# Kernel optimization log

Hardware: AMD Instinct MI355X
Metric: run time of the kernel (lower is better)

The kernel has to match this reference:

```python
import jax, jax.numpy as jnp
import numpy as np

# dims
A, V = 262, 100000          # alphabet, vocab
EC, HC = 64, 128            # char embed / char lstm hidden
EW, HW = 300, 512           # word embed / word lstm hidden
FC, OUT = 512, 20           # fc dim / num classes
S, L = 2048, 16             # words per sentence, chars per word
DW = EW + 2 * HC            # word-lstm input dim = 556


def _lstm_final(x, Wih, Whh, bih, bhh):
    """Run a unidirectional LSTM over x: [T, B, E]; return final hidden [B, H].
    Gate order (torch): i, f, g, o. c' = sig(f)*c + sig(i)*tanh(g); h = sig(o)*tanh(c')."""
    B = x.shape[1]
    H = Whh.shape[1]
    # precompute input projections for all timesteps: [T, B, 4H]
    xz = jnp.einsum('tbe,ge->tbg', x, Wih) + bih

    def step(carry, xz_t):
        h, c = carry
        z = xz_t + h @ Whh.T + bhh
        i, f, g, o = jnp.split(z, 4, axis=-1)
        c = jax.nn.sigmoid(f) * c + jax.nn.sigmoid(i) * jnp.tanh(g)
        h = jax.nn.sigmoid(o) * jnp.tanh(c)
        return (h, c), None

    init = (jnp.zeros((B, H), x.dtype), jnp.zeros((B, H), x.dtype))
    (h, _), _ = jax.lax.scan(step, init, xz)
    return h


def _bilstm_final(x, pf, pb):
    """Bidirectional LSTM final hidden states, concatenated: [B, 2H].
    Matches torch's hidden_state.view(-1, 2H) for num_layers=1."""
    hf = _lstm_final(x, *pf)
    hb = _lstm_final(x[::-1], *pb)
    return jnp.concatenate([hf, hb], axis=-1)


def setup_inputs() -> dict:
    key = jax.random.key(0)
    ks = jax.random.split(key, 24)
    n = lambda k, shp: (jax.random.normal(k, shp, dtype=jnp.float32) * 0.05)
    inp = {
        'sentence_c': jax.random.randint(ks[0], (S, L), 0, A),
        'sentence_w': jax.random.randint(ks[1], (S,), 0, V),
        'char_emb': n(ks[2], (A, EC)),
        'cWih_f': n(ks[3], (4 * HC, EC)), 'cWhh_f': n(ks[4], (4 * HC, HC)),
        'cbih_f': n(ks[5], (4 * HC,)),    'cbhh_f': n(ks[6], (4 * HC,)),
        'cWih_b': n(ks[7], (4 * HC, EC)), 'cWhh_b': n(ks[8], (4 * HC, HC)),
        'cbih_b': n(ks[9], (4 * HC,)),    'cbhh_b': n(ks[10], (4 * HC,)),
        'word_emb': n(ks[11], (V, EW)),
        'wWih_f': n(ks[12], (4 * HW, DW)), 'wWhh_f': n(ks[13], (4 * HW, HW)),
        'wbih_f': n(ks[14], (4 * HW,)),    'wbhh_f': n(ks[15], (4 * HW,)),
        'wWih_b': n(ks[16], (4 * HW, DW)), 'wWhh_b': n(ks[17], (4 * HW, HW)),
        'wbih_b': n(ks[18], (4 * HW,)),    'wbhh_b': n(ks[19], (4 * HW,)),
        'fc1_w': n(ks[20], (FC, 2 * HW)), 'fc1_b': n(ks[21], (FC,)),
        'fc2_w': n(ks[22], (OUT, FC)),    'fc2_b': n(ks[23], (OUT,)),
    }
    return inp


def reference(sentence_c, sentence_w, char_emb,
              cWih_f, cWhh_f, cbih_f, cbhh_f, cWih_b, cWhh_b, cbih_b, cbhh_b,
              word_emb,
              wWih_f, wWhh_f, wbih_f, wbhh_f, wWih_b, wWhh_b, wbih_b, wbhh_b,
              fc1_w, fc1_b, fc2_w, fc2_b):
    # --- per-word char BiLSTM, batched over all S words at once ---
    ce = char_emb[sentence_c]                 # [S, L, EC]
    ce = jnp.transpose(ce, (1, 0, 2))         # [L, S, EC] : time-major, words as batch
    char_enc = _bilstm_final(ce,
                             (cWih_f, cWhh_f, cbih_f, cbhh_f),
                             (cWih_b, cWhh_b, cbih_b, cbhh_b))  # [S, 2*HC]
    # --- word-level BiLSTM over the sentence (batch 1) ---
    we = word_emb[sentence_w]                 # [S, EW]
    wc = jnp.concatenate([we, char_enc], axis=-1)[:, None, :]   # [S, 1, DW]
    h = _bilstm_final(wc,
                      (wWih_f, wWhh_f, wbih_f, wbhh_f),
                      (wWih_b, wWhh_b, wbih_b, wbhh_b))         # [1, 2*HW]
    # --- classifier head ---
    z = jax.nn.relu(h @ fc1_w.T + fc1_b)
    z = z @ fc2_w.T + fc2_b
    return jax.nn.softmax(z, axis=-1)         # [1, OUT]
```

## Files before the change

kernel.cpp:

```cpp
#include <hip/hip_runtime.h>
#include <math.h>

#define SDIM 2048
#define LDIM 16
#define ECD 64
#define HCD 128
#define EWD 300
#define HWD 512
#define DWD 556
#define FCD 512
#define OUTD 20

typedef unsigned int uint32;

static constexpr int OFF_CWIHT = 0;
static constexpr int OFF_CWHHT = 65536;
static constexpr int OFF_CENC  = 196608;
static constexpr int OFF_WC    = 720896;
static constexpr int OFF_H     = 1859584;
static constexpr int OFF_HFIN  = 3957760;

#define SENT 0xFFFFFFFFu
#define HSLOT 1049088

__device__ __forceinline__ float sigmoidf_(float x) {
    return 1.0f / (1.0f + __expf(-x));
}
__device__ __forceinline__ float tanhf_(float x) {
    x = fminf(10.0f, fmaxf(-10.0f, x));
    float e2 = __expf(2.0f * x);
    return (e2 - 1.0f) / (e2 + 1.0f);
}

__global__ void k0_prep(const float* __restrict__ cWih_f, const float* __restrict__ cWhh_f,
                        const float* __restrict__ cWih_b, const float* __restrict__ cWhh_b,
                        float* __restrict__ ws) {
    const int nt = gridDim.x * blockDim.x;
    const int t0 = blockIdx.x * blockDim.x + threadIdx.x;
    float* cWihT = ws + OFF_CWIHT;
    float* cWhhT = ws + OFF_CWHHT;
    uint32* hT = (uint32*)(ws + OFF_H);
    for (int i = t0; i < 2 * 512 * 64; i += nt) {
        int d = i / (512 * 64), rem = i % (512 * 64);
        int r = rem / 64, k = rem % 64;
        const float* src = d ? cWih_b : cWih_f;
        cWihT[(d * 64 + k) * 512 + r] = src[r * 64 + k];
    }
    for (int i = t0; i < 2 * 512 * 128; i += nt) {
        int d = i / (512 * 128), rem = i % (512 * 128);
        int r = rem / 128, k = rem % 128;
        const float* src = d ? cWhh_b : cWhh_f;
        cWhhT[(d * 128 + k) * 512 + r] = src[r * 128 + k];
    }
    for (int i = t0; i < 2 * HSLOT; i += nt) {
        int rel = i % HSLOT;
        hT[i] = (rel < 512) ? 0u : SENT;
    }
}

__global__ __launch_bounds__(256) void k1_charlstm(
        const int* __restrict__ sc, const float* __restrict__ cemb,
        float* __restrict__ ws,
        const float* __restrict__ cbih_f, const float* __restrict__ cbhh_f,
        const float* __restrict__ cbih_b, const float* __restrict__ cbhh_b) {
    const int tid = threadIdx.x;
    const int dir = blockIdx.x >> 8;
    const int w0 = (blockIdx.x & 255) * 8;
    const float* WihT = ws + OFF_CWIHT + dir * 64 * 512;
    const float* WhhT = ws + OFF_CWHHT + dir * 128 * 512;
    float* char_enc = ws + OFF_CENC;
    const float* bih = dir ? cbih_b : cbih_f;
    const float* bhh = dir ? cbhh_b : cbhh_f;

    __shared__ __align__(16) float x_lds[8][64];
    __shared__ __align__(16) float h_lds[8][128];
    __shared__ float fo_lds[2][8][128];

    const int r0 = tid, r1 = tid + 256;
    const float bz0 = bih[r0] + bhh[r0];
    const float bz1 = bih[r1] + bhh[r1];

    for (int i = tid; i < 8 * 128; i += 256) ((float*)h_lds)[i] = 0.0f;
    float c[8];
#pragma unroll
    for (int w = 0; w < 8; w++) c[w] = 0.0f;
    __syncthreads();

    for (int t = 0; t < 16; t++) {
        const int tx = dir ? (15 - t) : t;
        {
            int w = tid >> 6, e = tid & 63;
            int i0 = sc[(w0 + w) * 16 + tx];
            x_lds[w][e] = cemb[i0 * 64 + e];
            int i1 = sc[(w0 + w + 4) * 16 + tx];
            x_lds[w + 4][e] = cemb[i1 * 64 + e];
        }
        __syncthreads();

        float a0[8], a1[8];
#pragma unroll
        for (int w = 0; w < 8; w++) { a0[w] = bz0; a1[w] = bz1; }

        for (int k = 0; k < 64; k += 4) {
            float w00 = WihT[(k + 0) * 512 + r0], w01 = WihT[(k + 1) * 512 + r0];
            float w02 = WihT[(k + 2) * 512 + r0], w03 = WihT[(k + 3) * 512 + r0];
            float w10 = WihT[(k + 0) * 512 + r1], w11 = WihT[(k + 1) * 512 + r1];
            float w12 = WihT[(k + 2) * 512 + r1], w13 = WihT[(k + 3) * 512 + r1];
#pragma unroll
            for (int w = 0; w < 8; w++) {
                float4 xq = *(const float4*)&x_lds[w][k];
                a0[w] += w00 * xq.x + w01 * xq.y + w02 * xq.z + w03 * xq.w;
                a1[w] += w10 * xq.x + w11 * xq.y + w12 * xq.z + w13 * xq.w;
            }
        }
        for (int k = 0; k < 128; k += 4) {
            float w00 = WhhT[(k + 0) * 512 + r0], w01 = WhhT[(k + 1) * 512 + r0];
            float w02 = WhhT[(k + 2) * 512 + r0], w03 = WhhT[(k + 3) * 512 + r0];
            float w10 = WhhT[(k + 0) * 512 + r1], w11 = WhhT[(k + 1) * 512 + r1];
            float w12 = WhhT[(k + 2) * 512 + r1], w13 = WhhT[(k + 3) * 512 + r1];
#pragma unroll
            for (int w = 0; w < 8; w++) {
                float4 hq = *(const float4*)&h_lds[w][k];
                a0[w] += w00 * hq.x + w01 * hq.y + w02 * hq.z + w03 * hq.w;
                a1[w] += w10 * hq.x + w11 * hq.y + w12 * hq.z + w13 * hq.w;
            }
        }
        if (tid >= 128) {
            int e = tid - 128;
#pragma unroll
            for (int w = 0; w < 8; w++) { fo_lds[0][w][e] = a0[w]; fo_lds[1][w][e] = a1[w]; }
        }
        __syncthreads();
        if (tid < 128) {
            int e = tid;
#pragma unroll
            for (int w = 0; w < 8; w++) {
                float zi = a0[w], zg = a1[w];
                float zf = fo_lds[0][w][e], zo = fo_lds[1][w][e];
                float cn = sigmoidf_(zf) * c[w] + sigmoidf_(zi) * tanhf_(zg);
                c[w] = cn;
                h_lds[w][e] = sigmoidf_(zo) * tanhf_(cn);
            }
        }
        __syncthreads();
    }
    if (tid < 128) {
        int e = tid;
        for (int w = 0; w < 8; w++)
            char_enc[(w0 + w) * 256 + dir * 128 + e] = h_lds[w][e];
    }
}

__global__ void k2_wc(const int* __restrict__ sw, const float* __restrict__ wemb,
                      float* __restrict__ ws) {
    const int t = blockIdx.x;
    const int tid = threadIdx.x;
    const float* char_enc = ws + OFF_CENC;
    float* wc = ws + OFF_WC;
    const int widx = sw[t];
    for (int k = tid; k < 300; k += 256) wc[t * 556 + k] = wemb[widx * 300 + k];
    for (int k = tid; k < 256; k += 256) wc[t * 556 + 300 + k] = char_enc[t * 256 + k];
}

__global__ __launch_bounds__(256, 1) void k4_wordlstm(
        const float* __restrict__ wWih_f, const float* __restrict__ wWhh_f,
        const float* __restrict__ wbih_f, const float* __restrict__ wbhh_f,
        const float* __restrict__ wWih_b, const float* __restrict__ wWhh_b,
        const float* __restrict__ wbih_b, const float* __restrict__ wbhh_b,
        float* __restrict__ ws) {
    const int tid = threadIdx.x;
    const int w = tid >> 6;
    const int lane = tid & 63;
    const int dir = blockIdx.x >> 6;
    const int slice = blockIdx.x & 63;
    const int E0 = slice * 8;
    const int r = lane >> 3, s = lane & 7;
    const int q = r >> 1, e = r & 1;
    const int elem = E0 + 2 * w + e;
    const int grow = q * 512 + elem;

    const float* Wih = dir ? wWih_b : wWih_f;
    const float* Whh = dir ? wWhh_b : wWhh_f;
    const float* bih = dir ? wbih_b : wbih_f;
    const float* bhh = dir ? wbhh_b : wbhh_f;
    const float* wc = ws + OFF_WC;
    uint32* hT = (uint32*)(ws + OFF_H) + (size_t)dir * HSLOT;
    float* hfin = ws + OFF_HFIN;

    const float bz = bih[grow] + bhh[grow];
    const float bzs = (s == 0) ? bz : 0.0f;

    float4 wr[16];
#pragma unroll
    for (int j = 0; j < 16; j++)
        wr[j] = *(const float4*)&Whh[grow * 512 + (s + 8 * j) * 4];
    float4 wih[18];
#pragma unroll
    for (int cj = 0; cj < 18; cj++) {
        int cc = s + 8 * cj;
        if (cc < 139) wih[cj] = *(const float4*)&Wih[grow * 556 + cc * 4];
        else { wih[cj].x = wih[cj].y = wih[cj].z = wih[cj].w = 0.0f; }
    }

    __shared__ __align__(16) uint32 hbuf[2][512];
    __shared__ int flag[2];

    if (tid < 2) flag[tid] = 0;
    __syncthreads();

    float cstate = 0.0f;
    const int eh = lane >> 5;

    float acc_ih = bzs;
    {
        const float* wcrow = wc + (dir ? 2047 : 0) * 556;
#pragma unroll
        for (int cj = 0; cj < 18; cj++) {
            int cc = s + 8 * cj;
            if (cc < 139) {
                float4 b = *(const float4*)&wcrow[cc * 4];
                acc_ih += wih[cj].x * b.x + wih[cj].y * b.y + wih[cj].z * b.z + wih[cj].w * b.w;
            }
        }
    }

    for (int t = 0; t < 2048; t++) {
        const int par = t & 1;
        if (w == 0) {
            uint32* hs = hT + (size_t)t * 512;
            uint32 v[8];
            while (true) {
#pragma unroll
                for (int m = 0; m < 8; m++)
                    v[m] = __hip_atomic_load(&hs[lane + 64 * m], __ATOMIC_RELAXED, __HIP_MEMORY_SCOPE_AGENT);
                uint32 bad = 0;
#pragma unroll
                for (int m = 0; m < 8; m++) bad |= (v[m] == SENT) ? 1u : 0u;
                if (!__any(bad)) break;
            }
            uint32* bufp = hbuf[par];
#pragma unroll
            for (int m = 0; m < 8; m++) bufp[lane + 64 * m] = v[m];
            asm volatile("s_waitcnt lgkmcnt(0)" ::: "memory");
            if (lane == 0) *(volatile int*)&flag[par] = t + 1;
        } else {
            while (*(volatile int*)&flag[par] < t + 1) { }
            asm volatile("" ::: "memory");
        }
        float acc = acc_ih;
        {
            const float* hb = (const float*)hbuf[par];
#pragma unroll
            for (int j = 0; j < 16; j++) {
                float4 hq = *(const float4*)&hb[(s + 8 * j) * 4];
                acc += wr[j].x * hq.x + wr[j].y * hq.y + wr[j].z * hq.z + wr[j].w * hq.w;
            }
        }
        acc += __shfl_xor(acc, 1);
        acc += __shfl_xor(acc, 2);
        acc += __shfl_xor(acc, 4);
        float zi = __shfl(acc, 8 * eh);
        float zf = __shfl(acc, 16 + 8 * eh);
        float zg = __shfl(acc, 32 + 8 * eh);
        float zo = __shfl(acc, 48 + 8 * eh);
        float cn = sigmoidf_(zf) * cstate + sigmoidf_(zi) * tanhf_(zg);
        cstate = cn;
        float hv = sigmoidf_(zo) * tanhf_(cn);
        if ((lane & 31) == 0) {
            int eidx = E0 + 2 * w + eh;
            __hip_atomic_store(&hT[(size_t)(t + 1) * 512 + eidx], __float_as_uint(hv),
                               __ATOMIC_RELAXED, __HIP_MEMORY_SCOPE_AGENT);
            if (t == 2047) hfin[dir * 512 + eidx] = hv;
        }
        if (t < 2047) {
            acc_ih = bzs;
            const float* wcrow = wc + (size_t)(dir ? (2046 - t) : (t + 1)) * 556;
#pragma unroll
            for (int cj = 0; cj < 18; cj++) {
                int cc = s + 8 * cj;
                if (cc < 139) {
                    float4 b = *(const float4*)&wcrow[cc * 4];
                    acc_ih += wih[cj].x * b.x + wih[cj].y * b.y + wih[cj].z * b.z + wih[cj].w * b.w;
                }
            }
        }
    }
}

__global__ __launch_bounds__(256) void k5_head(
        const float* __restrict__ ws,
        const float* __restrict__ fc1_w, const float* __restrict__ fc1_b,
        const float* __restrict__ fc2_w, const float* __restrict__ fc2_b,
        float* __restrict__ out) {
    __shared__ float hl[1024];
    __shared__ float z1[512];
    __shared__ float z2[20];
    const int tid = threadIdx.x;
    const float* hfin = ws + OFF_HFIN;
    for (int i = tid; i < 1024; i += 256) hl[i] = hfin[i];
    __syncthreads();
    for (int o = tid; o < 512; o += 256) {
        float a = fc1_b[o];
        const float* wrow = fc1_w + o * 1024;
        for (int k = 0; k < 1024; k++) a += wrow[k] * hl[k];
        z1[o] = fmaxf(a, 0.0f);
    }
    __syncthreads();
    if (tid < 20) {
        float a = fc2_b[tid];
        const float* wrow = fc2_w + tid * 512;
        for (int k = 0; k < 512; k++) a += wrow[k] * z1[k];
        z2[tid] = a;
    }
    __syncthreads();
    if (tid == 0) {
        float m = -1e30f;
        for (int i = 0; i < 20; i++) m = fmaxf(m, z2[i]);
        float sum = 0.0f, ex[20];
        for (int i = 0; i < 20; i++) { ex[i] = __expf(z2[i] - m); sum += ex[i]; }
        for (int i = 0; i < 20; i++) out[i] = ex[i] / sum;
    }
}

extern "C" void kernel_launch(void* const* d_in, const int* in_sizes, int n_in,
                              void* d_out, int out_size, void* d_ws, size_t ws_size,
                              hipStream_t stream) {
    const int*   sc     = (const int*)d_in[0];
    const int*   sw     = (const int*)d_in[1];
    const float* cemb   = (const float*)d_in[2];
    const float* cWih_f = (const float*)d_in[3];
    const float* cWhh_f = (const float*)d_in[4];
    const float* cbih_f = (const float*)d_in[5];
    const float* cbhh_f = (const float*)d_in[6];
    const float* cWih_b = (const float*)d_in[7];
    const float* cWhh_b = (const float*)d_in[8];
    const float* cbih_b = (const float*)d_in[9];
    const float* cbhh_b = (const float*)d_in[10];
    const float* wemb   = (const float*)d_in[11];
    const float* wWih_f = (const float*)d_in[12];
    const float* wWhh_f = (const float*)d_in[13];
    const float* wbih_f = (const float*)d_in[14];
    const float* wbhh_f = (const float*)d_in[15];
    const float* wWih_b = (const float*)d_in[16];
    const float* wWhh_b = (const float*)d_in[17];
    const float* wbih_b = (const float*)d_in[18];
    const float* wbhh_b = (const float*)d_in[19];
    const float* fc1_w  = (const float*)d_in[20];
    const float* fc1_b  = (const float*)d_in[21];
    const float* fc2_w  = (const float*)d_in[22];
    const float* fc2_b  = (const float*)d_in[23];
    float* ws = (float*)d_ws;
    float* out = (float*)d_out;

    k0_prep<<<256, 256, 0, stream>>>(cWih_f, cWhh_f, cWih_b, cWhh_b, ws);
    k1_charlstm<<<512, 256, 0, stream>>>(sc, cemb, ws, cbih_f, cbhh_f, cbih_b, cbhh_b);
    k2_wc<<<2048, 256, 0, stream>>>(sw, wemb, ws);
    k4_wordlstm<<<128, 256, 0, stream>>>(wWih_f, wWhh_f, wbih_f, wbhh_f,
                                         wWih_b, wWhh_b, wbih_b, wbhh_b, ws);
    k5_head<<<1, 256, 0, stream>>>(ws, fc1_w, fc1_b, fc2_w, fc2_b, out);
}
```

Before: 4.412 ms.

## Add dedicated producer wavefront to poll global hidden state in word LSTM

```diff
diff --git a/kernel.cpp b/kernel.cpp
--- a/kernel.cpp
+++ b/kernel.cpp
@@ -162,7 +162,7 @@
     for (int k = tid; k < 256; k += 256) wc[t * 556 + 300 + k] = char_enc[t * 256 + k];
 }
 
-__global__ __launch_bounds__(256, 1) void k4_wordlstm(
+__global__ __launch_bounds__(320, 1) void k4_wordlstm(
         const float* __restrict__ wWih_f, const float* __restrict__ wWhh_f,
         const float* __restrict__ wbih_f, const float* __restrict__ wbhh_f,
         const float* __restrict__ wWih_b, const float* __restrict__ wWhh_b,
@@ -174,6 +174,64 @@
     const int dir = blockIdx.x >> 6;
     const int slice = blockIdx.x & 63;
     const int E0 = slice * 8;
+
+    const float* wc = ws + OFF_WC;
+    uint32* hT = (uint32*)(ws + OFF_H) + (size_t)dir * HSLOT;
+    float* hfin = ws + OFF_HFIN;
+
+    __shared__ __align__(16) uint32 hbuf[2][512];
+    __shared__ int flag[2];
+
+    if (tid < 2) flag[tid] = 0;
+    __syncthreads();
+
+    if (w == 4) {
+        const int b0 = 4 * lane;
+        const int b1 = 256 + 4 * lane;
+        for (int t = 0; t < 2048; t++) {
+            const int par = t & 1;
+            uint32* hs = hT + (size_t)t * 512;
+            uint4 a, b;
+            bool ok = false;
+            for (int round = 0; round < 4; round++) {
+                asm volatile(
+                    "global_load_dwordx4 %0, %2, off sc0 sc1\n\t"
+                    "global_load_dwordx4 %1, %3, off sc0 sc1\n\t"
+                    "s_waitcnt vmcnt(0)"
+                    : "=&v"(a), "=&v"(b)
+                    : "v"(&hs[b0]), "v"(&hs[b1])
+                    : "memory");
+                uint32 bad = (a.x == SENT) | (a.y == SENT) | (a.z == SENT) | (a.w == SENT)
+                           | (b.x == SENT) | (b.y == SENT) | (b.z == SENT) | (b.w == SENT);
+                if (!__any(bad)) { ok = true; break; }
+            }
+            if (!ok) {
+                while (true) {
+                    uint32 v[8];
+#pragma unroll
+                    for (int m = 0; m < 4; m++)
+                        v[m] = __hip_atomic_load(&hs[b0 + m], __ATOMIC_RELAXED, __HIP_MEMORY_SCOPE_AGENT);
+#pragma unroll
+                    for (int m = 0; m < 4; m++)
+                        v[4 + m] = __hip_atomic_load(&hs[b1 + m], __ATOMIC_RELAXED, __HIP_MEMORY_SCOPE_AGENT);
+                    uint32 bad = 0;
+#pragma unroll
+                    for (int m = 0; m < 8; m++) bad |= (v[m] == SENT) ? 1u : 0u;
+                    if (!__any(bad)) {
+                        a.x = v[0]; a.y = v[1]; a.z = v[2]; a.w = v[3];
+                        b.x = v[4]; b.y = v[5]; b.z = v[6]; b.w = v[7];
+                        break;
+                    }
+                }
+            }
+            *(uint4*)&hbuf[par][b0] = a;
+            *(uint4*)&hbuf[par][b1] = b;
+            asm volatile("s_waitcnt lgkmcnt(0)" ::: "memory");
+            if (lane == 0) *(volatile int*)&flag[par] = t + 1;
+        }
+        return;
+    }
+
     const int r = lane >> 3, s = lane & 7;
     const int q = r >> 1, e = r & 1;
     const int elem = E0 + 2 * w + e;
@@ -183,9 +241,6 @@
     const float* Whh = dir ? wWhh_b : wWhh_f;
     const float* bih = dir ? wbih_b : wbih_f;
     const float* bhh = dir ? wbhh_b : wbhh_f;
-    const float* wc = ws + OFF_WC;
-    uint32* hT = (uint32*)(ws + OFF_H) + (size_t)dir * HSLOT;
-    float* hfin = ws + OFF_HFIN;
 
     const float bz = bih[grow] + bhh[grow];
     const float bzs = (s == 0) ? bz : 0.0f;
@@ -202,18 +257,12 @@
         else { wih[cj].x = wih[cj].y = wih[cj].z = wih[cj].w = 0.0f; }
     }
 
-    __shared__ __align__(16) uint32 hbuf[2][512];
-    __shared__ int flag[2];
-
-    if (tid < 2) flag[tid] = 0;
-    __syncthreads();
-
     float cstate = 0.0f;
     const int eh = lane >> 5;
 
     float acc_ih = bzs;
     {
-        const float* wcrow = wc + (dir ? 2047 : 0) * 556;
+        const float* wcrow = wc + (size_t)(dir ? 2047 : 0) * 556;
 #pragma unroll
         for (int cj = 0; cj < 18; cj++) {
             int cc = s + 8 * cj;
@@ -226,27 +275,8 @@
 
     for (int t = 0; t < 2048; t++) {
         const int par = t & 1;
-        if (w == 0) {
-            uint32* hs = hT + (size_t)t * 512;
-            uint32 v[8];
-            while (true) {
-#pragma unroll
-                for (int m = 0; m < 8; m++)
-                    v[m] = __hip_atomic_load(&hs[lane + 64 * m], __ATOMIC_RELAXED, __HIP_MEMORY_SCOPE_AGENT);
-                uint32 bad = 0;
-#pragma unroll
-                for (int m = 0; m < 8; m++) bad |= (v[m] == SENT) ? 1u : 0u;
-                if (!__any(bad)) break;
-            }
-            uint32* bufp = hbuf[par];
-#pragma unroll
-            for (int m = 0; m < 8; m++) bufp[lane + 64 * m] = v[m];
-            asm volatile("s_waitcnt lgkmcnt(0)" ::: "memory");
-            if (lane == 0) *(volatile int*)&flag[par] = t + 1;
-        } else {
-            while (*(volatile int*)&flag[par] < t + 1) { }
-            asm volatile("" ::: "memory");
-        }
+        while (*(volatile int*)&flag[par] < t + 1) { }
+        asm volatile("" ::: "memory");
         float acc = acc_ih;
         {
             const float* hb = (const float*)hbuf[par];
@@ -355,7 +385,7 @@
     k0_prep<<<256, 256, 0, stream>>>(cWih_f, cWhh_f, cWih_b, cWhh_b, ws);
     k1_charlstm<<<512, 256, 0, stream>>>(sc, cemb, ws, cbih_f, cbhh_f, cbih_b, cbhh_b);
     k2_wc<<<2048, 256, 0, stream>>>(sw, wemb, ws);
-    k4_wordlstm<<<128, 256, 0, stream>>>(wWih_f, wWhh_f, wbih_f, wbhh_f,
+    k4_wordlstm<<<128, 320, 0, stream>>>(wWih_f, wWhh_f, wbih_f, wbhh_f,
                                          wWih_b, wWhh_b, wbih_b, wbhh_b, ws);
     k5_head<<<1, 256, 0, stream>>>(ws, fc1_w, fc1_b, fc2_w, fc2_b, out);
 }
```

After: 6.162 ms. 39.7% more time.
